# Performance work log

Hardware: AMD Instinct MI355X
Metric: run time of the kernel (lower is better)

Reference implementation:

```python
import jax, jax.numpy as jnp
import numpy as np

DIM, DEPTH, DH, H, NLAT, MAXT, MAXF, FFM = 1024, 6, 64, 8, 64, 8, 16, 4
INNER = DH * H

def _ln(x, w, b, eps=1e-5):
    m = jnp.mean(x, axis=-1, keepdims=True)
    v = jnp.mean(jnp.square(x - m), axis=-1, keepdims=True)
    return (x - m) * jax.lax.rsqrt(v + eps) * w + b

def setup_inputs() -> dict:
    key = jax.random.key(0)
    ks = iter(jax.random.split(key, 32))
    s = 0.02
    d = {
        'x': jax.random.normal(next(ks), (2, 8, 16, 256, DIM), jnp.float32),
        'latents': jax.random.normal(next(ks), (NLAT, DIM), jnp.float32),
        'frame_emb': jax.random.normal(next(ks), (MAXF, DIM), jnp.float32),
        'media_emb': jax.random.normal(next(ks), (MAXT, 1, DIM), jnp.float32),
        'lnm_w': jnp.ones((DEPTH, DIM)), 'lnm_b': jnp.zeros((DEPTH, DIM)),
        'lnl_w': jnp.ones((DEPTH, DIM)), 'lnl_b': jnp.zeros((DEPTH, DIM)),
        'Wq': jax.random.normal(next(ks), (DEPTH, DIM, INNER), jnp.float32) * s,
        'Wkv': jax.random.normal(next(ks), (DEPTH, DIM, 2 * INNER), jnp.float32) * s,
        'Wo': jax.random.normal(next(ks), (DEPTH, INNER, DIM), jnp.float32) * s,
        'ffln_w': jnp.ones((DEPTH, DIM)), 'ffln_b': jnp.zeros((DEPTH, DIM)),
        'W1': jax.random.normal(next(ks), (DEPTH, DIM, FFM * DIM), jnp.float32) * s,
        'b1': jnp.zeros((DEPTH, FFM * DIM)),
        'W2': jax.random.normal(next(ks), (DEPTH, FFM * DIM, DIM), jnp.float32) * s,
        'b2': jnp.zeros((DEPTH, DIM)),
        'fln_w': jnp.ones((DIM,)), 'fln_b': jnp.zeros((DIM,)),
    }
    return d

def _split_heads(t):  # b T n (h d) -> b h T n d
    b, T, n, _ = t.shape
    return t.reshape(b, T, n, H, DH).transpose(0, 3, 1, 2, 4)

def _forward(x, latents, frame_emb, media_emb, lnm_w, lnm_b, lnl_w, lnl_b,
             Wq, Wkv, Wo, ffln_w, ffln_b, W1, b1, W2, b2, fln_w, fln_b):
    b, T, F, v, d = x.shape
    x = x + frame_emb[:F][None, None, :, None, :]      # b T F v d
    x = x.reshape(b, T, F * v, d)
    x = x + media_emb[:T]                              # [T,1,d] broadcasts
    lat = jnp.broadcast_to(latents, (b, T, NLAT, d))
    scale = DH ** -0.5
    for i in range(DEPTH):
        xn = _ln(x, lnm_w[i], lnm_b[i])
        ln_lat = _ln(lat, lnl_w[i], lnl_b[i])
        q = _split_heads(ln_lat @ Wq[i]) * scale       # b h T n2 dh
        kv = jnp.concatenate([xn, ln_lat], axis=2) @ Wkv[i]
        k, vv = jnp.split(kv, 2, axis=-1)
        k, vv = _split_heads(k), _split_heads(vv)      # b h T (n1+n2) dh
        sim = jnp.einsum('bhtid,bhtjd->bhtij', q, k)
        sim = sim - jax.lax.stop_gradient(jnp.max(sim, axis=-1, keepdims=True))
        attn = jax.nn.softmax(sim, axis=-1)
        o = jnp.einsum('bhtij,bhtjd->bhtid', attn, vv)
        o = o.transpose(0, 2, 3, 1, 4).reshape(b, T, NLAT, INNER)
        lat = (o @ Wo[i]) + lat
        h = _ln(lat, ffln_w[i], ffln_b[i])
        h = jax.nn.gelu(h @ W1[i] + b1[i], approximate=False) @ W2[i] + b2[i]
        lat = h + lat
    return _ln(lat, fln_w, fln_b)

def reference(x, latents, frame_emb, media_emb, lnm_w, lnm_b, lnl_w, lnl_b,
              Wq, Wkv, Wo, ffln_w, ffln_b, W1, b1, W2, b2, fln_w, fln_b):
    return _forward(x, latents, frame_emb, media_emb, lnm_w, lnm_b, lnl_w, lnl_b,
                    Wq, Wkv, Wo, ffln_w, ffln_b, W1, b1, W2, b2, fln_w, fln_b)
```

## Files before the change

kernel.cpp:

```cpp
#include <hip/hip_runtime.h>
#include <math.h>


#define DIM   1024
#define DEPTH 6
#define HEADS 8
#define NLAT  64
#define INNER 512
#define FFD   4096
#define XROWS 65536
#define LROWS 1024
#define NBT   16
#define QKVN  1536

typedef __attribute__((ext_vector_type(8))) short bf16x8;
typedef __attribute__((ext_vector_type(4))) float f32x4;

#define WAITV(n) asm volatile("s_waitcnt vmcnt(" #n ")" ::: "memory")

__device__ __forceinline__ short f2bf(float f) {
  union { float f; unsigned u; } v; v.f = f;
  unsigned r = v.u + 0x7fffu + ((v.u >> 16) & 1u);
  return (short)(r >> 16);
}

__device__ __forceinline__ void gload16(const void* g, void* l) {
  __builtin_amdgcn_global_load_lds(
      (const __attribute__((address_space(1))) unsigned int*)g,
      (__attribute__((address_space(3))) unsigned int*)l, 16, 0, 0);
}

__device__ __forceinline__ f32x4 zero_f4() { f32x4 z; z[0]=0.f; z[1]=0.f; z[2]=0.f; z[3]=0.f; return z; }
__device__ __forceinline__ bf16x8 zero_b8() { bf16x8 z;
#pragma unroll
  for (int e=0;e<8;e++) z[e]=0; return z; }

__global__ __launch_bounds__(256)
void prep_kernel(const float* __restrict__ x, const float* __restrict__ fe,
                 const float* __restrict__ me, short* __restrict__ xhat)
{
  int lane = threadIdx.x & 63;
  int r = blockIdx.x*4 + (threadIdx.x >> 6);
  int f = (r >> 8) & 15, tt = (r >> 12) & 7;
  const float4* xp = (const float4*)(x + (size_t)r*DIM);
  const float4* fp = (const float4*)(fe + (size_t)f*DIM);
  const float4* mp = (const float4*)(me + (size_t)tt*DIM);
  float y[16];
  float s = 0.f, sq = 0.f;
#pragma unroll
  for (int k = 0; k < 4; k++) {
    float4 xv = xp[k*64 + lane], fv = fp[k*64 + lane], mv = mp[k*64 + lane];
    float a0 = xv.x+fv.x+mv.x, a1 = xv.y+fv.y+mv.y, a2 = xv.z+fv.z+mv.z, a3 = xv.w+fv.w+mv.w;
    y[k*4+0]=a0; y[k*4+1]=a1; y[k*4+2]=a2; y[k*4+3]=a3;
    s += a0+a1+a2+a3; sq += a0*a0+a1*a1+a2*a2+a3*a3;
  }
#pragma unroll
  for (int off = 32; off >= 1; off >>= 1) {
    s  += __shfl_xor(s,  off, 64);
    sq += __shfl_xor(sq, off, 64);
  }
  float mean = s * (1.0f/DIM);
  float var  = sq * (1.0f/DIM) - mean*mean;
  float rs = rsqrtf(var + 1e-5f);
  short4* op = (short4*)(xhat + (size_t)r*DIM);
#pragma unroll
  for (int k = 0; k < 4; k++) {
    short4 o;
    o.x = f2bf((y[k*4+0]-mean)*rs); o.y = f2bf((y[k*4+1]-mean)*rs);
    o.z = f2bf((y[k*4+2]-mean)*rs); o.w = f2bf((y[k*4+3]-mean)*rs);
    op[k*64 + lane] = o;
  }
}

__device__ __forceinline__ void reduce2(float& s, float& sq, float* sh) {
#pragma unroll
  for (int off = 32; off >= 1; off >>= 1) {
    s  += __shfl_xor(s,  off, 64);
    sq += __shfl_xor(sq, off, 64);
  }
  int t = threadIdx.x;
  if ((t & 63) == 0) { sh[(t >> 6)*2] = s; sh[(t >> 6)*2 + 1] = sq; }
  __syncthreads();
  s  = sh[0] + sh[2] + sh[4] + sh[6];
  sq = sh[1] + sh[3] + sh[5] + sh[7];
}

template<bool OBF>
__global__ __launch_bounds__(256)
void ln_kernel(const float* __restrict__ in, const float* __restrict__ w,
               const float* __restrict__ b, void* __restrict__ outp)
{
  __shared__ float sh[8];
  int r = blockIdx.x, t = threadIdx.x;
  float4 xv = ((const float4*)(in + (size_t)r*DIM))[t];
  float s = xv.x+xv.y+xv.z+xv.w;
  float sq = xv.x*xv.x+xv.y*xv.y+xv.z*xv.z+xv.w*xv.w;
  reduce2(s, sq, sh);
  float mean = s*(1.0f/DIM), var = sq*(1.0f/DIM) - mean*mean;
  float rs = rsqrtf(var + 1e-5f);
  float4 wv = ((const float4*)w)[t], bv = ((const float4*)b)[t];
  float o0 = (xv.x-mean)*rs*wv.x + bv.x;
  float o1 = (xv.y-mean)*rs*wv.y + bv.y;
  float o2 = (xv.z-mean)*rs*wv.z + bv.z;
  float o3 = (xv.w-mean)*rs*wv.w + bv.w;
  if (OBF) {
    short4 o; o.x=f2bf(o0); o.y=f2bf(o1); o.z=f2bf(o2); o.w=f2bf(o3);
    ((short4*)((short*)outp + (size_t)r*DIM))[t] = o;
  } else {
    float4 o; o.x=o0; o.y=o1; o.z=o2; o.w=o3;
    ((float4*)((float*)outp + (size_t)r*DIM))[t] = o;
  }
}

__global__ __launch_bounds__(256)
void latinit_ln_kernel(const float* __restrict__ latents, const float* __restrict__ w,
                       const float* __restrict__ b, float* __restrict__ lat,
                       short* __restrict__ lnlat)
{
  __shared__ float sh[8];
  int r = blockIdx.x, t = threadIdx.x;
  int i = r & 63;
  float4 a = ((const float4*)(latents + (size_t)i*DIM))[t];
  ((float4*)(lat + (size_t)r*DIM))[t] = a;
  float s = a.x+a.y+a.z+a.w;
  float sq = a.x*a.x+a.y*a.y+a.z*a.z+a.w*a.w;
  reduce2(s, sq, sh);
  float mean = s*(1.0f/DIM), var = sq*(1.0f/DIM) - mean*mean;
  float rs = rsqrtf(var + 1e-5f);
  float4 wv = ((const float4*)w)[t], bv = ((const float4*)b)[t];
  short4 o;
  o.x = f2bf((a.x-mean)*rs*wv.x + bv.x);
  o.y = f2bf((a.y-mean)*rs*wv.y + bv.y);
  o.z = f2bf((a.z-mean)*rs*wv.z + bv.z);
  o.w = f2bf((a.w-mean)*rs*wv.w + bv.w);
  ((short4*)(lnlat + (size_t)r*DIM))[t] = o;
}

__global__ __launch_bounds__(256)
void kvbp_kernel(const float* __restrict__ lnm_b, const float* __restrict__ Wkv,
                 float* __restrict__ kvb_part)
{
  int z = blockIdx.x, i = blockIdx.y, t = threadIdx.x;
  const float* W = Wkv + (size_t)i*DIM*DIM;
  const float* bv = lnm_b + (size_t)i*DIM;
  float acc0=0,acc1=0,acc2=0,acc3=0;
  for (int k = z*64; k < z*64+64; k++) {
    float b = bv[k];
    const float* Wr = W + (size_t)k*DIM;
    acc0 += b * Wr[t];       acc1 += b * Wr[t+256];
    acc2 += b * Wr[t+512];   acc3 += b * Wr[t+768];
  }
  float* o = kvb_part + (size_t)(i*16 + z)*DIM;
  o[t] = acc0; o[t+256] = acc1; o[t+512] = acc2; o[t+768] = acc3;
}

__global__ __launch_bounds__(256)
void kvbred_kernel(const float* __restrict__ kvb_part, float* __restrict__ kvb)
{
  int i = blockIdx.x, t = threadIdx.x;
#pragma unroll
  for (int j = 0; j < 4; j++) {
    int col = t + j*256;
    float s = 0.f;
#pragma unroll
    for (int z = 0; z < 16; z++) s += kvb_part[(size_t)(i*16 + z)*DIM + col];
    kvb[i*DIM + col] = s;
  }
}

__global__ __launch_bounds__(256)
void tcast_all_kernel(const float* __restrict__ Wkv, const float* __restrict__ Wq,
                      const float* __restrict__ Wo, const float* __restrict__ W1,
                      const float* __restrict__ W2, const float* __restrict__ lnmw,
                      short* __restrict__ Wkv_f, short* __restrict__ qkvW,
                      short* __restrict__ Wo_h, short* __restrict__ W1_h,
                      short* __restrict__ W2_h)
{
  int b = blockIdx.x;
  const float* src; short* dst; const float* fold = nullptr; float scale = 1.0f;
  int K, N, bx, ntx;
  if (b < 256)      { src=Wkv; dst=Wkv_f; fold=lnmw; K=1024; N=1024; bx=b;      ntx=16; }
  else if (b < 384) { src=Wq;  dst=qkvW;  scale=0.125f; K=1024; N=512; bx=b-256; ntx=8; }
  else if (b < 640) { src=Wkv; dst=qkvW+512*1024; K=1024; N=1024; bx=b-384; ntx=16; }
  else if (b < 768) { src=Wo;  dst=Wo_h;  K=512;  N=1024; bx=b-640; ntx=16; }
  else if (b < 1792){ src=W1;  dst=W1_h;  K=1024; N=4096; bx=b-768; ntx=64; }
  else              { src=W2;  dst=W2_h;  K=4096; N=1024; bx=b-1792; ntx=16; }
  int n0 = (bx % ntx)*64, k0 = (bx / ntx)*64;
  __shared__ float tile[64][65];
  int t = threadIdx.x;
#pragma unroll
  for (int i = 0; i < 16; i++) {
    int rr = (t >> 6) + i*4, cc = t & 63;
    float v = src[(size_t)(k0+rr)*N + n0 + cc] * scale;
    if (fold) v *= fold[k0 + rr];
    tile[rr][cc] = v;
  }
  __syncthreads();
#pragma unroll
  for (int i = 0; i < 16; i++) {
    int nn = (t >> 6) + i*4, kk = t & 63;
    dst[(size_t)(n0+nn)*K + k0 + kk] = f2bf(tile[kk][nn]);
  }
}

__global__ __launch_bounds__(512, 1)
void gemm256p_kernel(const short* __restrict__ A, const short* __restrict__ Bt,
                     short* __restrict__ C, const float* __restrict__ bias,
                     int M, int N, int K)
{
  __shared__ __align__(16) short lds[65536];
  char* ldsc = (char*)lds;
  const int t = threadIdx.x, lane = t & 63, wid = t >> 6;
  const int wm = wid >> 2, wn = wid & 3;

  const int nwg = gridDim.x * gridDim.y;
  const int id = blockIdx.y * gridDim.x + blockIdx.x;
  const int work = (id & 7) * (nwg >> 3) + (id >> 3);
  const int bn = work % gridDim.x, bm = work / gridDim.x;
  const int m0 = bm * 256, n0 = bn * 256;

  f32x4 acc[8][4];
#pragma unroll
  for (int m=0;m<8;m++)
#pragma unroll
    for (int n=0;n<4;n++) acc[m][n] = zero_f4();

  const int hK = K << 7;
  const short* pA[2]; const short* pB[2]; int ldst[2];
#pragma unroll
  for (int i = 0; i < 2; i++) {
    int chunk = i*512 + t;
    int rh = chunk >> 3, sl = chunk & 7;
    int ss = sl ^ (rh & 7);
    pA[i] = A + (size_t)(m0 + rh)*K + ss*8;
    pB[i] = Bt + (size_t)(n0 + rh)*K + ss*8;
    ldst[i] = (i*512 + (wid << 6))*16;
  }
  auto stage = [&](int tile, int mat, int half) {
    char* dbase = ldsc + mat*65536 + (tile & 1)*32768 + half*16384;
#pragma unroll
    for (int i = 0; i < 2; i++) {
      const short* src = (mat ? pB[i] : pA[i]) + half*hK + tile*64;
      gload16(src, dbase + ldst[i]);
    }
  };

  const int sk0 = (((lane >> 4)    ) ^ (lane & 7)) * 16;
  const int sk1 = ((4 + (lane >> 4)) ^ (lane & 7)) * 16;
  const int rowb = (lane & 15) * 128;
  const char* aB[2] = { ldsc + wm*16384 + rowb + sk0, ldsc + wm*16384 + rowb + sk1 };
  const char* bB[2] = { ldsc + 65536 + wn*8192 + rowb + sk0, ldsc + 65536 + wn*8192 + rowb + sk1 };

#define PHASE(BUF, Q, STAGE_STMT, GATE) do {                               \
    if ((Q) == 0) {                                                        \
      _Pragma("unroll") for (int n_=0;n_<4;n_++)                           \
        _Pragma("unroll") for (int k_=0;k_<2;k_++)                         \
          bfr[n_][k_] = *(const bf16x8*)(bB[k_] + (BUF)*32768 + n_*2048);  \
    }                                                                      \
    _Pragma("unroll") for (int i_=0;i_<2;i_++)                             \
      _Pragma("unroll") for (int k_=0;k_<2;k_++)                           \
        afr[i_][k_] = *(const bf16x8*)(aB[k_] + (BUF)*32768 + (2*(Q)+i_)*2048); \
    STAGE_STMT;                                                            \
    GATE;                                                                  \
    __builtin_amdgcn_sched_barrier(0);                                     \
    __builtin_amdgcn_s_barrier();                                          \
    asm volatile("s_waitcnt lgkmcnt(0)" ::: "memory");                     \
    __builtin_amdgcn_sched_barrier(0);                                     \
    __builtin_amdgcn_s_setprio(1);                                         \
    _Pragma("unroll") for (int k_=0;k_<2;k_++)                             \
      _Pragma("unroll") for (int i_=0;i_<2;i_++)                           \
        _Pragma("unroll") for (int n_=0;n_<4;n_++)                         \
          acc[2*(Q)+i_][n_] = __builtin_amdgcn_mfma_f32_16x16x32_bf16(     \
              afr[i_][k_], bfr[n_][k_], acc[2*(Q)+i_][n_], 0, 0, 0);       \
    __builtin_amdgcn_s_setprio(0);                                         \
    __builtin_amdgcn_sched_barrier(0);                                     \
    __builtin_amdgcn_s_barrier();                                          \
  } while (0)

  const int NU = K >> 7;
  stage(0, 0, 0); stage(0, 0, 1); stage(0, 1, 0); stage(0, 1, 1);
  stage(1, 1, 0); stage(1, 1, 1);
  WAITV(4);
  __builtin_amdgcn_sched_barrier(0);
  __builtin_amdgcn_s_barrier();

#pragma unroll 1
  for (int u = 0; u < NU; ++u) {
    const int t0 = 2*u, t1 = t0 + 1;
    const bool more = (u + 1 < NU);
    bf16x8 bfr[4][2], afr[2][2];
    PHASE(0, 0, stage(t1, 0, 0),               (void)0);
    PHASE(0, 1, stage(t1, 0, 1),               (void)0);
    PHASE(0, 2, if (more) stage(t0+2, 1, 0),   (void)0);
    PHASE(0, 3, if (more) stage(t0+2, 1, 1),   if (more) { WAITV(4); } else { WAITV(0); });
    PHASE(1, 0, if (more) stage(t0+2, 0, 0),   (void)0);
    PHASE(1, 1, if (more) stage(t0+2, 0, 1),   (void)0);
    PHASE(1, 2, if (more) stage(t1+2, 1, 0),   (void)0);
    PHASE(1, 3, if (more) stage(t1+2, 1, 1),   if (more) { WAITV(4); });
  }
#undef PHASE

  const int g = lane >> 4;
#pragma unroll
  for (int m=0;m<8;m++) {
#pragma unroll
    for (int n=0;n<4;n++) {
#pragma unroll
      for (int r=0;r<4;r++) {
        int mm = m0 + wm*128 + m*16 + g*4 + r;
        int nn = n0 + wn*64 + n*16 + (lane & 15);
        float v = acc[m][n][r] + bias[nn];
        C[(size_t)mm*N + nn] = f2bf(v);
      }
    }
  }
}

template<int EPI, bool HAS_BIAS>
__global__ __launch_bounds__(256, 2)
void gemm_kernel(const short* __restrict__ A, const short* __restrict__ Bt,
                 void* __restrict__ Cout, const float* __restrict__ bias,
                 int M, int N, int K, int ldk)
{
  __shared__ __align__(16) short As[128*64];
  __shared__ __align__(16) short Bs[128*64];
  const int t = threadIdx.x;
  const int lane = t & 63, w = t >> 6;
  const int m0 = blockIdx.x * 128, n0 = blockIdx.y * 128;
  const int wr = (w >> 1) * 64, wc = (w & 1) * 64;
  const short* Ap = A + (size_t)blockIdx.z * K;
  const short* Btp = Bt + (size_t)blockIdx.z * K;

  f32x4 acc[4][4];
#pragma unroll
  for (int i=0;i<4;i++)
#pragma unroll
    for (int j=0;j<4;j++) acc[i][j] = zero_f4();

  for (int kt = 0; kt < K; kt += 64) {
#pragma unroll
    for (int i = 0; i < 4; i++) {
      int chunk = i*256 + t;
      int row = chunk >> 3, slot = chunk & 7;
      int ss = slot ^ (row & 7);
      gload16(Ap + (size_t)(m0 + row)*ldk + kt + ss*8,
              (char*)As + (i*256 + (w<<6))*16);
    }
#pragma unroll
    for (int i = 0; i < 4; i++) {
      int chunk = i*256 + t;
      int row = chunk >> 3, slot = chunk & 7;
      int ss = slot ^ (row & 7);
      gload16(Btp + (size_t)(n0 + row)*ldk + kt + ss*8,
              (char*)Bs + (i*256 + (w<<6))*16);
    }
    __syncthreads();

#pragma unroll
    for (int ks = 0; ks < 2; ks++) {
      bf16x8 af[4], bfr[4];
#pragma unroll
      for (int i=0;i<4;i++) {
        int row = wr + i*16 + (lane & 15);
        int slot = (ks*4 + (lane >> 4)) ^ (row & 7);
        af[i] = *(const bf16x8*)((const char*)As + row*128 + slot*16);
        int nrow = wc + i*16 + (lane & 15);
        int nslot = (ks*4 + (lane >> 4)) ^ (nrow & 7);
        bfr[i] = *(const bf16x8*)((const char*)Bs + nrow*128 + nslot*16);
      }
#pragma unroll
      for (int i=0;i<4;i++)
#pragma unroll
        for (int j=0;j<4;j++)
          acc[i][j] = __builtin_amdgcn_mfma_f32_16x16x32_bf16(af[i], bfr[j], acc[i][j], 0, 0, 0);
    }
    __syncthreads();
  }

  const int g = lane >> 4;
#pragma unroll
  for (int i=0;i<4;i++) {
#pragma unroll
    for (int j=0;j<4;j++) {
#pragma unroll
      for (int r=0;r<4;r++) {
        int m = m0 + wr + i*16 + g*4 + r;
        int n = n0 + wc + j*16 + (lane & 15);
        float v = acc[i][j][r];
        if (EPI == 0) {
          if (HAS_BIAS) v += bias[n];
          ((short*)Cout)[(size_t)m*N + n] = f2bf(v);
        } else if (EPI == 1) {
          if (HAS_BIAS) v += bias[n];
          float gl = 0.5f * v * (1.0f + erff(v * 0.70710678f));
          ((short*)Cout)[(size_t)m*N + n] = f2bf(gl);
        } else if (EPI == 2) {
          if (HAS_BIAS) v += bias[n];
          float* o = (float*)Cout + (size_t)m*N + n;
          *o += v;
        } else {
          ((float*)Cout)[(size_t)blockIdx.z*M*N + (size_t)m*N + n] = v;
        }
      }
    }
  }
}

template<bool LAST>
__global__ __launch_bounds__(256)
void w2red_ln_kernel(const float* __restrict__ part, const float* __restrict__ b2,
                     float* __restrict__ lat, const float* __restrict__ w,
                     const float* __restrict__ bb, void* __restrict__ dst)
{
  __shared__ float sh[8];
  int r = blockIdx.x, t = threadIdx.x;
  int idx = r*256 + t;
  float4 a = ((float4*)lat)[idx];
  float4 b4 = ((const float4*)b2)[t];
  a.x += b4.x; a.y += b4.y; a.z += b4.z; a.w += b4.w;
#pragma unroll
  for (int z = 0; z < 4; z++) {
    float4 p = ((const float4*)(part + (size_t)z*LROWS*DIM))[idx];
    a.x += p.x; a.y += p.y; a.z += p.z; a.w += p.w;
  }
  ((float4*)lat)[idx] = a;
  float s = a.x+a.y+a.z+a.w;
  float sq = a.x*a.x+a.y*a.y+a.z*a.z+a.w*a.w;
  reduce2(s, sq, sh);
  float mean = s*(1.0f/DIM), var = sq*(1.0f/DIM) - mean*mean;
  float rs = rsqrtf(var + 1e-5f);
  float4 wv = ((const float4*)w)[t], bv = ((const float4*)bb)[t];
  float o0 = (a.x-mean)*rs*wv.x + bv.x;
  float o1 = (a.y-mean)*rs*wv.y + bv.y;
  float o2 = (a.z-mean)*rs*wv.z + bv.z;
  float o3 = (a.w-mean)*rs*wv.w + bv.w;
  if (LAST) {
    float4 o; o.x=o0; o.y=o1; o.z=o2; o.w=o3;
    ((float4*)((float*)dst + (size_t)r*DIM))[t] = o;
  } else {
    short4 o; o.x=f2bf(o0); o.y=f2bf(o1); o.z=f2bf(o2); o.w=f2bf(o3);
    ((short4*)((short*)dst + (size_t)r*DIM))[t] = o;
  }
}

__global__ __launch_bounds__(256, 2)
void attn_part_kernel(const short* __restrict__ qkvlat, const short* __restrict__ kvbuf,
                      float* __restrict__ part_O, float* __restrict__ part_m,
                      float* __restrict__ part_l)
{
  __shared__ __align__(16) short q_sh[64*64];
  __shared__ __align__(16) short K_sh[128*64];
  __shared__ __align__(16) short VT_sh[64*128];
  __shared__ __align__(16) short P_sh[64*132];

  const int t = threadIdx.x, lane = t & 63, w = t >> 6;
  const int bid = blockIdx.x;
  const int s = bid & 7, bh = bid >> 3;
  const int h = bh & 7, bt = bh >> 3;

  {
    const short* qsrc = qkvlat + (size_t)(bt*64)*QKVN + h*64;
#pragma unroll
    for (int i = 0; i < 2; i++) {
      int chunk = i*256 + t;
      int row = chunk >> 3, slot = chunk & 7;
      gload16(qsrc + (size_t)row*QKVN + ((slot ^ (row & 7))*8),
              (char*)q_sh + (i*256 + (w<<6))*16);
    }
  }

  float m_run[4], l_run[4];
#pragma unroll
  for (int r=0;r<4;r++){ m_run[r] = -1e30f; l_run[r] = 0.f; }
  f32x4 oacc[4];
#pragma unroll
  for (int j=0;j<4;j++) oacc[j] = zero_f4();

  const int nch = (s == 7) ? 5 : 4;
  for (int c5 = 0; c5 < nch; c5++) {
    __syncthreads();
    const bool isLat = (c5 == 4);
    const int jv = isLat ? 4 : 8;
    const short* kbase; int kstride, valid;
    if (!isLat) {
      kbase = kvbuf + ((size_t)bt*4096 + (s*4 + c5)*128)*DIM + h*64;
      kstride = DIM; valid = 128;
    } else {
      kbase = qkvlat + (size_t)(bt*64)*QKVN + 512 + h*64;
// ... 106 lines not shown
    for (int j=0;j<4;j++) {
#pragma unroll
      for (int r=0;r<4;r++)
        Ob[(rbase + r)*64 + j*16 + (lane & 15)] = oacc[j][r];
    }
    if ((lane & 15) == 0) {
#pragma unroll
      for (int r=0;r<4;r++) {
        part_m[(size_t)bid*64 + rbase + r] = m_run[r];
        part_l[(size_t)bid*64 + rbase + r] = l_run[r];
      }
    }
  }
}

__global__ __launch_bounds__(256)
void attn_combine_kernel(const float* __restrict__ part_O, const float* __restrict__ part_m,
                         const float* __restrict__ part_l, short* __restrict__ obuf)
{
  int bh = blockIdx.x, t = threadIdx.x;
  int q = t >> 2, c0 = (t & 3) * 16;
  int bt = bh >> 3, h = bh & 7;
  float m8[8], w8[8];
  float mmax = -1e30f;
#pragma unroll
  for (int s=0;s<8;s++) { m8[s] = part_m[(size_t)(bh*8+s)*64 + q]; mmax = fmaxf(mmax, m8[s]); }
  float lt = 0.f;
#pragma unroll
  for (int s=0;s<8;s++) { w8[s] = __expf(m8[s] - mmax); lt += w8[s] * part_l[(size_t)(bh*8+s)*64 + q]; }
  float inv = 1.0f / lt;
  float4 acc[4];
#pragma unroll
  for (int u=0;u<4;u++) { acc[u].x=0.f; acc[u].y=0.f; acc[u].z=0.f; acc[u].w=0.f; }
#pragma unroll
  for (int s=0;s<8;s++) {
    const float4* Ob = (const float4*)(part_O + ((size_t)(bh*8+s)*64 + q)*64 + c0);
#pragma unroll
    for (int u=0;u<4;u++) {
      float4 v = Ob[u];
      acc[u].x += w8[s]*v.x; acc[u].y += w8[s]*v.y;
      acc[u].z += w8[s]*v.z; acc[u].w += w8[s]*v.w;
    }
  }
  short* ob = obuf + (size_t)(bt*64 + q)*INNER + h*64 + c0;
#pragma unroll
  for (int u=0;u<4;u++) {
    short4 o;
    o.x = f2bf(acc[u].x*inv); o.y = f2bf(acc[u].y*inv);
    o.z = f2bf(acc[u].z*inv); o.w = f2bf(acc[u].w*inv);
    ((short4*)ob)[u] = o;
  }
}

extern "C" void kernel_launch(void* const* d_in, const int* in_sizes, int n_in,
                              void* d_out, int out_size, void* d_ws, size_t ws_size,
                              hipStream_t stream)
{
  (void)in_sizes; (void)n_in; (void)out_size; (void)ws_size;
  const float* x        = (const float*)d_in[0];
  const float* latents  = (const float*)d_in[1];
  const float* frame_e  = (const float*)d_in[2];
  const float* media_e  = (const float*)d_in[3];
  const float* lnm_w    = (const float*)d_in[4];
  const float* lnm_b    = (const float*)d_in[5];
  const float* lnl_w    = (const float*)d_in[6];
  const float* lnl_b    = (const float*)d_in[7];
  const float* Wq       = (const float*)d_in[8];
  const float* Wkv      = (const float*)d_in[9];
  const float* Wo       = (const float*)d_in[10];
  const float* ffln_w   = (const float*)d_in[11];
  const float* ffln_b   = (const float*)d_in[12];
  const float* W1       = (const float*)d_in[13];
  const float* b1       = (const float*)d_in[14];
  const float* W2       = (const float*)d_in[15];
  const float* b2       = (const float*)d_in[16];
  const float* fln_w    = (const float*)d_in[17];
  const float* fln_b    = (const float*)d_in[18];
  float* out = (float*)d_out;

  char* ws = (char*)d_ws;
  size_t off = 0;
  short* xhat   = (short*)(ws + off); off += (size_t)XROWS*DIM*2;
  short* kvbuf  = (short*)(ws + off); off += (size_t)XROWS*DIM*2;
  short* Wkv_f  = (short*)(ws + off); off += (size_t)DIM*DIM*2;
  short* qkvW   = (short*)(ws + off); off += (size_t)QKVN*DIM*2;
  short* Wo_h   = (short*)(ws + off); off += (size_t)INNER*DIM*2;
  short* W1_h   = (short*)(ws + off); off += (size_t)DIM*FFD*2;
  short* W2_h   = (short*)(ws + off); off += (size_t)FFD*DIM*2;
  float* kvb    = (float*)(ws + off); off += (size_t)DEPTH*DIM*4;
  float* kvbp   = (float*)(ws + off); off += (size_t)DEPTH*16*DIM*4;
  float* lat    = (float*)(ws + off); off += (size_t)LROWS*DIM*4;
  short* lnlat  = (short*)(ws + off); off += (size_t)LROWS*DIM*2;
  short* qkvlat = (short*)(ws + off); off += (size_t)LROWS*QKVN*2;
  short* obuf   = (short*)(ws + off); off += (size_t)LROWS*INNER*2;
  short* hbuf   = (short*)(ws + off); off += (size_t)LROWS*DIM*2;
  short* h1     = (short*)(ws + off); off += (size_t)LROWS*FFD*2;
  float* w2part = (float*)(ws + off); off += (size_t)4*LROWS*DIM*4;
  float* part_O = (float*)(ws + off); off += (size_t)1024*64*64*4;
  float* part_m = (float*)(ws + off); off += (size_t)1024*64*4;
  float* part_l = (float*)(ws + off); off += (size_t)1024*64*4;

  prep_kernel<<<XROWS/4, 256, 0, stream>>>(x, frame_e, media_e, xhat);
  latinit_ln_kernel<<<LROWS, 256, 0, stream>>>(latents, lnl_w, lnl_b, lat, lnlat);
  kvbp_kernel<<<dim3(16, DEPTH), 256, 0, stream>>>(lnm_b, Wkv, kvbp);
  kvbred_kernel<<<DEPTH, 256, 0, stream>>>(kvbp, kvb);

  for (int i = 0; i < DEPTH; i++) {
    tcast_all_kernel<<<2816, 256, 0, stream>>>(
        Wkv + (size_t)i*DIM*DIM, Wq + (size_t)i*DIM*INNER, Wo + (size_t)i*INNER*DIM,
        W1 + (size_t)i*DIM*FFD, W2 + (size_t)i*FFD*DIM, lnm_w + (size_t)i*DIM,
        Wkv_f, qkvW, Wo_h, W1_h, W2_h);

    gemm_kernel<0,false><<<dim3(LROWS/128, QKVN/128), 256, 0, stream>>>(
        lnlat, qkvW, qkvlat, nullptr, LROWS, QKVN, DIM, DIM);
    gemm256p_kernel<<<dim3(DIM/256, XROWS/256), 512, 0, stream>>>(
        xhat, Wkv_f, kvbuf, kvb + i*DIM, XROWS, DIM, DIM);
    attn_part_kernel<<<1024, 256, 0, stream>>>(qkvlat, kvbuf, part_O, part_m, part_l);
    attn_combine_kernel<<<128, 256, 0, stream>>>(part_O, part_m, part_l, obuf);
    gemm_kernel<2,false><<<dim3(LROWS/128, DIM/128), 256, 0, stream>>>(
        obuf, Wo_h, lat, nullptr, LROWS, DIM, INNER, INNER);
    ln_kernel<true><<<LROWS, 256, 0, stream>>>(lat, ffln_w + i*DIM, ffln_b + i*DIM, hbuf);
    gemm_kernel<1,true><<<dim3(LROWS/128, FFD/128), 256, 0, stream>>>(
        hbuf, W1_h, h1, b1 + (size_t)i*FFD, LROWS, FFD, DIM, DIM);
    gemm_kernel<4,false><<<dim3(LROWS/128, DIM/128, 4), 256, 0, stream>>>(
        h1, W2_h, w2part, nullptr, LROWS, DIM, DIM, FFD);
    if (i < DEPTH-1)
      w2red_ln_kernel<false><<<LROWS, 256, 0, stream>>>(
          w2part, b2 + (size_t)i*DIM, lat, lnl_w + (i+1)*DIM, lnl_b + (i+1)*DIM, lnlat);
    else
      w2red_ln_kernel<true><<<LROWS, 256, 0, stream>>>(
          w2part, b2 + (size_t)i*DIM, lat, fln_w, fln_b, out);
  }
}
```

Measured before the change: 2.077 ms.

## Double-buffer LDS fragment registers to overlap LDS reads with MFMA in GEMM

Restructures the GEMM main loop so the A and B fragments are ping-ponged between two register sets. The reads for the next phase are issued before the current phase's MFMAs, and the lgkmcnt waits are partial instead of full, so LDS read latency can hide behind matrix math. The WAITV gating is also moved earlier in the pipeline. In exchange, register pressure rises, the waitcnt accounting is subtle, and a miscount could race with the buffer stage writes.

```diff
diff --git a/kernel.cpp b/kernel.cpp
--- a/kernel.cpp
+++ b/kernel.cpp
@@ -248,33 +248,38 @@
   const int sk0 = (((lane >> 4)    ) ^ (lane & 7)) * 16;
   const int sk1 = ((4 + (lane >> 4)) ^ (lane & 7)) * 16;
   const int rowb = (lane & 15) * 128;
-  const char* aB[2] = { ldsc + wm*16384 + rowb + sk0, ldsc + wm*16384 + rowb + sk1 };
-  const char* bB[2] = { ldsc + 65536 + wn*8192 + rowb + sk0, ldsc + 65536 + wn*8192 + rowb + sk1 };
-
-#define PHASE(BUF, Q, STAGE_STMT, GATE) do {                               \
-    if ((Q) == 0) {                                                        \
-      _Pragma("unroll") for (int n_=0;n_<4;n_++)                           \
-        _Pragma("unroll") for (int k_=0;k_<2;k_++)                         \
-          bfr[n_][k_] = *(const bf16x8*)(bB[k_] + (BUF)*32768 + n_*2048);  \
-    }                                                                      \
-    _Pragma("unroll") for (int i_=0;i_<2;i_++)                             \
-      _Pragma("unroll") for (int k_=0;k_<2;k_++)                           \
-        afr[i_][k_] = *(const bf16x8*)(aB[k_] + (BUF)*32768 + (2*(Q)+i_)*2048); \
-    STAGE_STMT;                                                            \
-    GATE;                                                                  \
-    __builtin_amdgcn_sched_barrier(0);                                     \
-    __builtin_amdgcn_s_barrier();                                          \
-    asm volatile("s_waitcnt lgkmcnt(0)" ::: "memory");                     \
-    __builtin_amdgcn_sched_barrier(0);                                     \
-    __builtin_amdgcn_s_setprio(1);                                         \
-    _Pragma("unroll") for (int k_=0;k_<2;k_++)                             \
-      _Pragma("unroll") for (int i_=0;i_<2;i_++)                           \
-        _Pragma("unroll") for (int n_=0;n_<4;n_++)                         \
-          acc[2*(Q)+i_][n_] = __builtin_amdgcn_mfma_f32_16x16x32_bf16(     \
-              afr[i_][k_], bfr[n_][k_], acc[2*(Q)+i_][n_], 0, 0, 0);       \
-    __builtin_amdgcn_s_setprio(0);                                         \
-    __builtin_amdgcn_sched_barrier(0);                                     \
-    __builtin_amdgcn_s_barrier();                                          \
+  const char* aLB[2] = { ldsc + wm*16384 + rowb + sk0, ldsc + wm*16384 + rowb + sk1 };
+  const char* bLB[2] = { ldsc + 65536 + wn*8192 + rowb + sk0, ldsc + 65536 + wn*8192 + rowb + sk1 };
+
+  bf16x8 aA[2][2], aB[2][2];
+  bf16x8 bC[4][2], bN[4][2];
+
+#define RD_A(DST, BUF, Q)                                                   \
+  { _Pragma("unroll") for (int i_=0;i_<2;i_++)                              \
+      _Pragma("unroll") for (int k_=0;k_<2;k_++)                            \
+        DST[i_][k_] = *(const bf16x8*)(aLB[k_] + (BUF)*32768 + (2*(Q)+i_)*2048); }
+#define RD_B2(DST, BUF, N0)                                                 \
+  { _Pragma("unroll") for (int n_=0;n_<2;n_++)                              \
+      _Pragma("unroll") for (int k_=0;k_<2;k_++)                            \
+        DST[(N0)+n_][k_] = *(const bf16x8*)(bLB[k_] + (BUF)*32768 + ((N0)+n_)*2048); }
+
+#define PHASE(AF, BF, Q, READS, STAGE_STMT, GATE, LGKM) do {                \
+    READS;                                                                  \
+    STAGE_STMT;                                                             \
+    GATE;                                                                   \
+    __builtin_amdgcn_sched_barrier(0);                                      \
+    __builtin_amdgcn_s_barrier();                                           \
+    asm volatile("s_waitcnt lgkmcnt(" #LGKM ")" ::: "memory");              \
+    __builtin_amdgcn_sched_barrier(0);                                      \
+    __builtin_amdgcn_s_setprio(1);                                          \
+    _Pragma("unroll") for (int k_=0;k_<2;k_++)                              \
+      _Pragma("unroll") for (int i_=0;i_<2;i_++)                            \
+        _Pragma("unroll") for (int n_=0;n_<4;n_++)                          \
+          acc[2*(Q)+i_][n_] = __builtin_amdgcn_mfma_f32_16x16x32_bf16(      \
+              AF[i_][k_], BF[n_][k_], acc[2*(Q)+i_][n_], 0, 0, 0);          \
+    __builtin_amdgcn_s_setprio(0);                                          \
+    __builtin_amdgcn_sched_barrier(0);                                      \
+    __builtin_amdgcn_s_barrier();                                           \
   } while (0)
 
   const int NU = K >> 7;
@@ -283,22 +288,28 @@
   WAITV(4);
   __builtin_amdgcn_sched_barrier(0);
   __builtin_amdgcn_s_barrier();
+  RD_B2(bC, 0, 0); RD_B2(bC, 0, 2);
+  __builtin_amdgcn_sched_barrier(0);
 
 #pragma unroll 1
   for (int u = 0; u < NU; ++u) {
     const int t0 = 2*u, t1 = t0 + 1;
     const bool more = (u + 1 < NU);
-    bf16x8 bfr[4][2], afr[2][2];
-    PHASE(0, 0, stage(t1, 0, 0),               (void)0);
-    PHASE(0, 1, stage(t1, 0, 1),               (void)0);
-    PHASE(0, 2, if (more) stage(t0+2, 1, 0),   (void)0);
-    PHASE(0, 3, if (more) stage(t0+2, 1, 1),   if (more) { WAITV(4); } else { WAITV(0); });
-    PHASE(1, 0, if (more) stage(t0+2, 0, 0),   (void)0);
-    PHASE(1, 1, if (more) stage(t0+2, 0, 1),   (void)0);
-    PHASE(1, 2, if (more) stage(t1+2, 1, 0),   (void)0);
-    PHASE(1, 3, if (more) stage(t1+2, 1, 1),   if (more) { WAITV(4); });
+    PHASE(aA, bC, 0, { RD_A(aA,0,0); RD_A(aB,0,1); }, stage(t1,0,0), (void)0, 4);
+    PHASE(aB, bC, 1, { RD_A(aA,0,2); },               stage(t1,0,1), WAITV(4), 4);
+    PHASE(aA, bC, 2, { RD_A(aB,0,3); RD_B2(bN,1,0); }, if (more) stage(t0+2,1,0), (void)0, 8);
+    PHASE(aB, bC, 3, { RD_B2(bN,1,2); },               if (more) stage(t0+2,1,1),
+          if (more) { WAITV(4); } else { WAITV(0); }, 8);
+    PHASE(aA, bN, 0, { RD_A(aA,1,0); RD_A(aB,1,1); }, if (more) stage(t0+2,0,0), (void)0, 4);
+    PHASE(aB, bN, 1, { RD_A(aA,1,2); },               if (more) stage(t0+2,0,1),
+          if (more) { WAITV(4); }, 4);
+    PHASE(aA, bN, 2, { RD_A(aB,1,3); RD_B2(bC,0,0); }, if (more) stage(t1+2,1,0), (void)0, 8);
+    PHASE(aB, bN, 3, { RD_B2(bC,0,2); },               if (more) stage(t1+2,1,1),
+          if (more) { WAITV(4); }, 8);
   }
 #undef PHASE
+#undef RD_A
+#undef RD_B2
 
   const int g = lane >> 4;
 #pragma unroll
```

Result: no change. 2.096 ms (+0.9%).

## Make big KV GEMM persistent over N-tiles and batch weight casts

Applied to the files above, without the earlier changes.

The large x-by-Wkv GEMM now launches 256 blocks, each owning a 256-row M stripe. Each block walks all four 256-wide N tiles in one continuous K pipeline, writing and resetting its accumulators every 16 k-steps. This keeps the A stripe hot in cache and removes the per-tile prologue and epilogue pipeline drains. Separately, the six per-layer weight transpose/cast launches are merged into one upfront launch writing per-layer buffers. This costs more workspace, and w2part now aliases the part_O buffer.

```diff
diff --git a/kernel.cpp b/kernel.cpp
--- a/kernel.cpp
+++ b/kernel.cpp
@@ -169,22 +169,24 @@
 }
 
 __global__ __launch_bounds__(256)
-void tcast_all_kernel(const float* __restrict__ Wkv, const float* __restrict__ Wq,
-                      const float* __restrict__ Wo, const float* __restrict__ W1,
-                      const float* __restrict__ W2, const float* __restrict__ lnmw,
-                      short* __restrict__ Wkv_f, short* __restrict__ qkvW,
-                      short* __restrict__ Wo_h, short* __restrict__ W1_h,
-                      short* __restrict__ W2_h)
-{
-  int b = blockIdx.x;
+void tcast_all6_kernel(const float* __restrict__ Wkv, const float* __restrict__ Wq,
+                       const float* __restrict__ Wo, const float* __restrict__ W1,
+                       const float* __restrict__ W2, const float* __restrict__ lnm_w,
+                       short* __restrict__ Wkvf_a, short* __restrict__ qkvW_a,
+                       short* __restrict__ Wo_a, short* __restrict__ W1_a,
+                       short* __restrict__ W2_a)
+{
+  int L = blockIdx.x / 2816;
+  int b = blockIdx.x % 2816;
+  const float* lWkv = Wkv + (size_t)L*DIM*DIM;
   const float* src; short* dst; const float* fold = nullptr; float scale = 1.0f;
   int K, N, bx, ntx;
-  if (b < 256)      { src=Wkv; dst=Wkv_f; fold=lnmw; K=1024; N=1024; bx=b;      ntx=16; }
-  else if (b < 384) { src=Wq;  dst=qkvW;  scale=0.125f; K=1024; N=512; bx=b-256; ntx=8; }
-  else if (b < 640) { src=Wkv; dst=qkvW+512*1024; K=1024; N=1024; bx=b-384; ntx=16; }
-  else if (b < 768) { src=Wo;  dst=Wo_h;  K=512;  N=1024; bx=b-640; ntx=16; }
-  else if (b < 1792){ src=W1;  dst=W1_h;  K=1024; N=4096; bx=b-768; ntx=64; }
-  else              { src=W2;  dst=W2_h;  K=4096; N=1024; bx=b-1792; ntx=16; }
+  if (b < 256)      { src=lWkv; dst=Wkvf_a + (size_t)L*DIM*DIM; fold=lnm_w + (size_t)L*DIM; K=1024; N=1024; bx=b; ntx=16; }
+  else if (b < 384) { src=Wq + (size_t)L*DIM*INNER; dst=qkvW_a + (size_t)L*QKVN*DIM; scale=0.125f; K=1024; N=512; bx=b-256; ntx=8; }
+  else if (b < 640) { src=lWkv; dst=qkvW_a + (size_t)L*QKVN*DIM + (size_t)512*1024; K=1024; N=1024; bx=b-384; ntx=16; }
+  else if (b < 768) { src=Wo + (size_t)L*INNER*DIM; dst=Wo_a + (size_t)L*INNER*DIM; K=512;  N=1024; bx=b-640; ntx=16; }
+  else if (b < 1792){ src=W1 + (size_t)L*DIM*FFD; dst=W1_a + (size_t)L*DIM*FFD; K=1024; N=4096; bx=b-768; ntx=64; }
+  else              { src=W2 + (size_t)L*FFD*DIM; dst=W2_a + (size_t)L*FFD*DIM; K=4096; N=1024; bx=b-1792; ntx=16; }
   int n0 = (bx % ntx)*64, k0 = (bx / ntx)*64;
   __shared__ float tile[64][65];
   int t = threadIdx.x;
@@ -204,20 +206,18 @@
 }
 
 __global__ __launch_bounds__(512, 1)
-void gemm256p_kernel(const short* __restrict__ A, const short* __restrict__ Bt,
-                     short* __restrict__ C, const float* __restrict__ bias,
-                     int M, int N, int K)
+void gemm256pp_kernel(const short* __restrict__ A, const short* __restrict__ Bt,
+                      short* __restrict__ C, const float* __restrict__ bias)
 {
   __shared__ __align__(16) short lds[65536];
   char* ldsc = (char*)lds;
   const int t = threadIdx.x, lane = t & 63, wid = t >> 6;
   const int wm = wid >> 2, wn = wid & 3;
-
-  const int nwg = gridDim.x * gridDim.y;
-  const int id = blockIdx.y * gridDim.x + blockIdx.x;
-  const int work = (id & 7) * (nwg >> 3) + (id >> 3);
-  const int bn = work % gridDim.x, bm = work / gridDim.x;
-  const int m0 = bm * 256, n0 = bn * 256;
+  const int K = DIM, N = DIM;
+
+  const int b = blockIdx.x;
+  const int bm = (b & 7)*32 + (b >> 3);
+  const int m0 = bm * 256;
 
   f32x4 acc[8][4];
 #pragma unroll
@@ -226,21 +226,24 @@
     for (int n=0;n<4;n++) acc[m][n] = zero_f4();
 
   const int hK = K << 7;
-  const short* pA[2]; const short* pB[2]; int ldst[2];
+  const short* pA[2]; const short* pB0[2]; int ldst[2];
 #pragma unroll
   for (int i = 0; i < 2; i++) {
     int chunk = i*512 + t;
     int rh = chunk >> 3, sl = chunk & 7;
     int ss = sl ^ (rh & 7);
-    pA[i] = A + (size_t)(m0 + rh)*K + ss*8;
-    pB[i] = Bt + (size_t)(n0 + rh)*K + ss*8;
+    pA[i]  = A + (size_t)(m0 + rh)*K + ss*8;
+    pB0[i] = Bt + (size_t)rh*K + ss*8;
     ldst[i] = (i*512 + (wid << 6))*16;
   }
-  auto stage = [&](int tile, int mat, int half) {
-    char* dbase = ldsc + mat*65536 + (tile & 1)*32768 + half*16384;
+  auto stage = [&](int vt, int mat, int half) {
+    char* dbase = ldsc + mat*65536 + (vt & 1)*32768 + half*16384;
+    const int koff = (vt & 15)*64;
+    const size_t bout = (size_t)(vt >> 4)*256*K;
 #pragma unroll
     for (int i = 0; i < 2; i++) {
-      const short* src = (mat ? pB[i] : pA[i]) + half*hK + tile*64;
+      const short* src = mat ? (pB0[i] + bout + half*hK + koff)
+                             : (pA[i] + half*hK + koff);
       gload16(src, dbase + ldst[i]);
     }
   };
@@ -277,43 +280,45 @@
     __builtin_amdgcn_s_barrier();                                          \
   } while (0)
 
-  const int NU = K >> 7;
+  const int NVT = 64;
   stage(0, 0, 0); stage(0, 0, 1); stage(0, 1, 0); stage(0, 1, 1);
   stage(1, 1, 0); stage(1, 1, 1);
   WAITV(4);
   __builtin_amdgcn_sched_barrier(0);
   __builtin_amdgcn_s_barrier();
 
+  const int g = lane >> 4;
 #pragma unroll 1
-  for (int u = 0; u < NU; ++u) {
-    const int t0 = 2*u, t1 = t0 + 1;
-    const bool more = (u + 1 < NU);
+  for (int u = 0; u < 32; ++u) {
+    const int vt0 = 2*u, vt1 = vt0 + 1;
+    const bool more = (vt0 + 2 < NVT);
     bf16x8 bfr[4][2], afr[2][2];
-    PHASE(0, 0, stage(t1, 0, 0),               (void)0);
-    PHASE(0, 1, stage(t1, 0, 1),               (void)0);
-    PHASE(0, 2, if (more) stage(t0+2, 1, 0),   (void)0);
-    PHASE(0, 3, if (more) stage(t0+2, 1, 1),   if (more) { WAITV(4); } else { WAITV(0); });
-    PHASE(1, 0, if (more) stage(t0+2, 0, 0),   (void)0);
-    PHASE(1, 1, if (more) stage(t0+2, 0, 1),   (void)0);
-    PHASE(1, 2, if (more) stage(t1+2, 1, 0),   (void)0);
-    PHASE(1, 3, if (more) stage(t1+2, 1, 1),   if (more) { WAITV(4); });
+    PHASE(0, 0, stage(vt1, 0, 0),               (void)0);
+    PHASE(0, 1, stage(vt1, 0, 1),               (void)0);
+    PHASE(0, 2, if (more) stage(vt0+2, 1, 0),   (void)0);
+    PHASE(0, 3, if (more) stage(vt0+2, 1, 1),   if (more) { WAITV(4); } else { WAITV(0); });
+    PHASE(1, 0, if (more) stage(vt0+2, 0, 0),   (void)0);
+    PHASE(1, 1, if (more) stage(vt0+2, 0, 1),   (void)0);
+    PHASE(1, 2, if (more) stage(vt1+2, 1, 0),   (void)0);
+    PHASE(1, 3, if (more) stage(vt1+2, 1, 1),   if (more) { WAITV(4); });
+    if ((u & 7) == 7) {
+      const int n0 = (u >> 3) * 256;
+#pragma unroll
+      for (int m=0;m<8;m++) {
+#pragma unroll
+        for (int n=0;n<4;n++) {
+#pragma unroll
+          for (int r=0;r<4;r++) {
+            int mm = m0 + wm*128 + m*16 + g*4 + r;
+            int nn = n0 + wn*64 + n*16 + (lane & 15);
+            C[(size_t)mm*N + nn] = f2bf(acc[m][n][r] + bias[nn]);
+          }
+          acc[m][n] = zero_f4();
+        }
+      }
+    }
   }
 #undef PHASE
-
-  const int g = lane >> 4;
-#pragma unroll
-  for (int m=0;m<8;m++) {
-#pragma unroll
-    for (int n=0;n<4;n++) {
-#pragma unroll
-      for (int r=0;r<4;r++) {
-        int mm = m0 + wm*128 + m*16 + g*4 + r;
-        int nn = n0 + wn*64 + n*16 + (lane & 15);
-        float v = acc[m][n][r] + bias[nn];
-        C[(size_t)mm*N + nn] = f2bf(v);
-      }
-    }
-  }
 }
 
 template<int EPI, bool HAS_BIAS>
@@ -676,11 +681,11 @@
   size_t off = 0;
   short* xhat   = (short*)(ws + off); off += (size_t)XROWS*DIM*2;
   short* kvbuf  = (short*)(ws + off); off += (size_t)XROWS*DIM*2;
-  short* Wkv_f  = (short*)(ws + off); off += (size_t)DIM*DIM*2;
-  short* qkvW   = (short*)(ws + off); off += (size_t)QKVN*DIM*2;
-  short* Wo_h   = (short*)(ws + off); off += (size_t)INNER*DIM*2;
-  short* W1_h   = (short*)(ws + off); off += (size_t)DIM*FFD*2;
-  short* W2_h   = (short*)(ws + off); off += (size_t)FFD*DIM*2;
+  short* Wkvf_a = (short*)(ws + off); off += (size_t)DEPTH*DIM*DIM*2;
+  short* qkvW_a = (short*)(ws + off); off += (size_t)DEPTH*QKVN*DIM*2;
+  short* Wo_a   = (short*)(ws + off); off += (size_t)DEPTH*INNER*DIM*2;
+  short* W1_a   = (short*)(ws + off); off += (size_t)DEPTH*DIM*FFD*2;
+  short* W2_a   = (short*)(ws + off); off += (size_t)DEPTH*FFD*DIM*2;
   float* kvb    = (float*)(ws + off); off += (size_t)DEPTH*DIM*4;
   float* kvbp   = (float*)(ws + off); off += (size_t)DEPTH*16*DIM*4;
   float* lat    = (float*)(ws + off); off += (size_t)LROWS*DIM*4;
@@ -689,8 +694,8 @@
   short* obuf   = (short*)(ws + off); off += (size_t)LROWS*INNER*2;
   short* hbuf   = (short*)(ws + off); off += (size_t)LROWS*DIM*2;
   short* h1     = (short*)(ws + off); off += (size_t)LROWS*FFD*2;
-  float* w2part = (float*)(ws + off); off += (size_t)4*LROWS*DIM*4;
   float* part_O = (float*)(ws + off); off += (size_t)1024*64*64*4;
+  float* w2part = part_O;
   float* part_m = (float*)(ws + off); off += (size_t)1024*64*4;
   float* part_l = (float*)(ws + off); off += (size_t)1024*64*4;
 
@@ -698,17 +703,19 @@
   latinit_ln_kernel<<<LROWS, 256, 0, stream>>>(latents, lnl_w, lnl_b, lat, lnlat);
   kvbp_kernel<<<dim3(16, DEPTH), 256, 0, stream>>>(lnm_b, Wkv, kvbp);
   kvbred_kernel<<<DEPTH, 256, 0, stream>>>(kvbp, kvb);
+  tcast_all6_kernel<<<DEPTH*2816, 256, 0, stream>>>(
+      Wkv, Wq, Wo, W1, W2, lnm_w, Wkvf_a, qkvW_a, Wo_a, W1_a, W2_a);
 
   for (int i = 0; i < DEPTH; i++) {
-    tcast_all_kernel<<<2816, 256, 0, stream>>>(
-        Wkv + (size_t)i*DIM*DIM, Wq + (size_t)i*DIM*INNER, Wo + (size_t)i*INNER*DIM,
-        W1 + (size_t)i*DIM*FFD, W2 + (size_t)i*FFD*DIM, lnm_w + (size_t)i*DIM,
-        Wkv_f, qkvW, Wo_h, W1_h, W2_h);
+    const short* Wkv_f = Wkvf_a + (size_t)i*DIM*DIM;
+    const short* qkvW  = qkvW_a + (size_t)i*QKVN*DIM;
+    const short* Wo_h  = Wo_a   + (size_t)i*INNER*DIM;
+    const short* W1_h  = W1_a   + (size_t)i*DIM*FFD;
+    const short* W2_h  = W2_a   + (size_t)i*FFD*DIM;
 
     gemm_kernel<0,false><<<dim3(LROWS/128, QKVN/128), 256, 0, stream>>>(
         lnlat, qkvW, qkvlat, nullptr, LROWS, QKVN, DIM, DIM);
-    gemm256p_kernel<<<dim3(DIM/256, XROWS/256), 512, 0, stream>>>(
-        xhat, Wkv_f, kvbuf, kvb + i*DIM, XROWS, DIM, DIM);
+    gemm256pp_kernel<<<256, 512, 0, stream>>>(xhat, Wkv_f, kvbuf, kvb + i*DIM);
     attn_part_kernel<<<1024, 256, 0, stream>>>(qkvlat, kvbuf, part_O, part_m, part_l);
     attn_combine_kernel<<<128, 256, 0, stream>>>(part_O, part_m, part_l, obuf);
     gemm_kernel<2,false><<<dim3(LROWS/128, DIM/128), 256, 0, stream>>>(
```

Result: slower. 2.192 ms (+5.5%).

## Hoist weight casts for all layers into one launch; split-K Wo with fused LN

Applied to the files above, without the earlier changes.

Weight transpose/cast work for all six layers now runs in a single large launch before the layer loop instead of one launch per layer, with per-layer bf16 weight buffers in the workspace. The Wo projection becomes a 2-way split-K GEMM writing partials. A new kernel sums those partials into the residual and applies the feed-forward LayerNorm in the same pass, replacing the separate accumulate epilogue and LN kernel. This raises parallelism for the small Wo GEMM and removes one launch and one pass over the latents, at the cost of more workspace and a larger upfront cast kernel. The W2 partial buffer now aliases the attention partial buffer.

```diff
diff --git a/kernel.cpp b/kernel.cpp
--- a/kernel.cpp
+++ b/kernel.cpp
@@ -83,33 +83,6 @@
   __syncthreads();
   s  = sh[0] + sh[2] + sh[4] + sh[6];
   sq = sh[1] + sh[3] + sh[5] + sh[7];
-}
-
-template<bool OBF>
-__global__ __launch_bounds__(256)
-void ln_kernel(const float* __restrict__ in, const float* __restrict__ w,
-               const float* __restrict__ b, void* __restrict__ outp)
-{
-  __shared__ float sh[8];
-  int r = blockIdx.x, t = threadIdx.x;
-  float4 xv = ((const float4*)(in + (size_t)r*DIM))[t];
-  float s = xv.x+xv.y+xv.z+xv.w;
-  float sq = xv.x*xv.x+xv.y*xv.y+xv.z*xv.z+xv.w*xv.w;
-  reduce2(s, sq, sh);
-  float mean = s*(1.0f/DIM), var = sq*(1.0f/DIM) - mean*mean;
-  float rs = rsqrtf(var + 1e-5f);
-  float4 wv = ((const float4*)w)[t], bv = ((const float4*)b)[t];
-  float o0 = (xv.x-mean)*rs*wv.x + bv.x;
-  float o1 = (xv.y-mean)*rs*wv.y + bv.y;
-  float o2 = (xv.z-mean)*rs*wv.z + bv.z;
-  float o3 = (xv.w-mean)*rs*wv.w + bv.w;
-  if (OBF) {
-    short4 o; o.x=f2bf(o0); o.y=f2bf(o1); o.z=f2bf(o2); o.w=f2bf(o3);
-    ((short4*)((short*)outp + (size_t)r*DIM))[t] = o;
-  } else {
-    float4 o; o.x=o0; o.y=o1; o.z=o2; o.w=o3;
-    ((float4*)((float*)outp + (size_t)r*DIM))[t] = o;
-  }
 }
 
 __global__ __launch_bounds__(256)
@@ -169,22 +142,24 @@
 }
 
 __global__ __launch_bounds__(256)
-void tcast_all_kernel(const float* __restrict__ Wkv, const float* __restrict__ Wq,
-                      const float* __restrict__ Wo, const float* __restrict__ W1,
-                      const float* __restrict__ W2, const float* __restrict__ lnmw,
-                      short* __restrict__ Wkv_f, short* __restrict__ qkvW,
-                      short* __restrict__ Wo_h, short* __restrict__ W1_h,
-                      short* __restrict__ W2_h)
-{
-  int b = blockIdx.x;
+void tcast_all6_kernel(const float* __restrict__ Wkv, const float* __restrict__ Wq,
+                       const float* __restrict__ Wo, const float* __restrict__ W1,
+                       const float* __restrict__ W2, const float* __restrict__ lnm_w,
+                       short* __restrict__ Wkvf_a, short* __restrict__ qkvW_a,
+                       short* __restrict__ Wo_a, short* __restrict__ W1_a,
+                       short* __restrict__ W2_a)
+{
+  int L = blockIdx.x / 2816;
+  int b = blockIdx.x % 2816;
+  const float* lWkv = Wkv + (size_t)L*DIM*DIM;
   const float* src; short* dst; const float* fold = nullptr; float scale = 1.0f;
   int K, N, bx, ntx;
-  if (b < 256)      { src=Wkv; dst=Wkv_f; fold=lnmw; K=1024; N=1024; bx=b;      ntx=16; }
-  else if (b < 384) { src=Wq;  dst=qkvW;  scale=0.125f; K=1024; N=512; bx=b-256; ntx=8; }
-  else if (b < 640) { src=Wkv; dst=qkvW+512*1024; K=1024; N=1024; bx=b-384; ntx=16; }
-  else if (b < 768) { src=Wo;  dst=Wo_h;  K=512;  N=1024; bx=b-640; ntx=16; }
-  else if (b < 1792){ src=W1;  dst=W1_h;  K=1024; N=4096; bx=b-768; ntx=64; }
-  else              { src=W2;  dst=W2_h;  K=4096; N=1024; bx=b-1792; ntx=16; }
+  if (b < 256)      { src=lWkv; dst=Wkvf_a + (size_t)L*DIM*DIM; fold=lnm_w + (size_t)L*DIM; K=1024; N=1024; bx=b; ntx=16; }
+  else if (b < 384) { src=Wq + (size_t)L*DIM*INNER; dst=qkvW_a + (size_t)L*QKVN*DIM; scale=0.125f; K=1024; N=512; bx=b-256; ntx=8; }
+  else if (b < 640) { src=lWkv; dst=qkvW_a + (size_t)L*QKVN*DIM + (size_t)512*1024; K=1024; N=1024; bx=b-384; ntx=16; }
+  else if (b < 768) { src=Wo + (size_t)L*INNER*DIM; dst=Wo_a + (size_t)L*INNER*DIM; K=512;  N=1024; bx=b-640; ntx=16; }
+  else if (b < 1792){ src=W1 + (size_t)L*DIM*FFD; dst=W1_a + (size_t)L*DIM*FFD; K=1024; N=4096; bx=b-768; ntx=64; }
+  else              { src=W2 + (size_t)L*FFD*DIM; dst=W2_a + (size_t)L*FFD*DIM; K=4096; N=1024; bx=b-1792; ntx=16; }
   int n0 = (bx % ntx)*64, k0 = (bx / ntx)*64;
   __shared__ float tile[64][65];
   int t = threadIdx.x;
@@ -394,16 +369,39 @@
           if (HAS_BIAS) v += bias[n];
           float gl = 0.5f * v * (1.0f + erff(v * 0.70710678f));
           ((short*)Cout)[(size_t)m*N + n] = f2bf(gl);
-        } else if (EPI == 2) {
-          if (HAS_BIAS) v += bias[n];
-          float* o = (float*)Cout + (size_t)m*N + n;
-          *o += v;
         } else {
           ((float*)Cout)[(size_t)blockIdx.z*M*N + (size_t)m*N + n] = v;
         }
       }
     }
   }
+}
+
+__global__ __launch_bounds__(256)
+void wored_ffln_kernel(const float* __restrict__ part, float* __restrict__ lat,
+                       const float* __restrict__ w, const float* __restrict__ bb,
+                       short* __restrict__ hbuf)
+{
+  __shared__ float sh[8];
+  int r = blockIdx.x, t = threadIdx.x;
+  int idx = r*256 + t;
+  float4 a = ((float4*)lat)[idx];
+  float4 p0 = ((const float4*)part)[idx];
+  float4 p1 = ((const float4*)(part + (size_t)LROWS*DIM))[idx];
+  a.x += p0.x + p1.x; a.y += p0.y + p1.y; a.z += p0.z + p1.z; a.w += p0.w + p1.w;
+  ((float4*)lat)[idx] = a;
+  float s = a.x+a.y+a.z+a.w;
+  float sq = a.x*a.x+a.y*a.y+a.z*a.z+a.w*a.w;
+  reduce2(s, sq, sh);
+  float mean = s*(1.0f/DIM), var = sq*(1.0f/DIM) - mean*mean;
+  float rs = rsqrtf(var + 1e-5f);
+  float4 wv = ((const float4*)w)[t], bv = ((const float4*)bb)[t];
+  short4 o;
+  o.x = f2bf((a.x-mean)*rs*wv.x + bv.x);
+  o.y = f2bf((a.y-mean)*rs*wv.y + bv.y);
+  o.z = f2bf((a.z-mean)*rs*wv.z + bv.z);
+  o.w = f2bf((a.w-mean)*rs*wv.w + bv.w);
+  ((short4*)(hbuf + (size_t)r*DIM))[t] = o;
 }
 
 template<bool LAST>
@@ -676,11 +674,11 @@
   size_t off = 0;
   short* xhat   = (short*)(ws + off); off += (size_t)XROWS*DIM*2;
   short* kvbuf  = (short*)(ws + off); off += (size_t)XROWS*DIM*2;
-  short* Wkv_f  = (short*)(ws + off); off += (size_t)DIM*DIM*2;
-  short* qkvW   = (short*)(ws + off); off += (size_t)QKVN*DIM*2;
-  short* Wo_h   = (short*)(ws + off); off += (size_t)INNER*DIM*2;
-  short* W1_h   = (short*)(ws + off); off += (size_t)DIM*FFD*2;
-  short* W2_h   = (short*)(ws + off); off += (size_t)FFD*DIM*2;
+  short* Wkvf_a = (short*)(ws + off); off += (size_t)DEPTH*DIM*DIM*2;
+  short* qkvW_a = (short*)(ws + off); off += (size_t)DEPTH*QKVN*DIM*2;
+  short* Wo_a   = (short*)(ws + off); off += (size_t)DEPTH*INNER*DIM*2;
+  short* W1_a   = (short*)(ws + off); off += (size_t)DEPTH*DIM*FFD*2;
+  short* W2_a   = (short*)(ws + off); off += (size_t)DEPTH*FFD*DIM*2;
   float* kvb    = (float*)(ws + off); off += (size_t)DEPTH*DIM*4;
   float* kvbp   = (float*)(ws + off); off += (size_t)DEPTH*16*DIM*4;
   float* lat    = (float*)(ws + off); off += (size_t)LROWS*DIM*4;
@@ -689,8 +687,9 @@
   short* obuf   = (short*)(ws + off); off += (size_t)LROWS*INNER*2;
   short* hbuf   = (short*)(ws + off); off += (size_t)LROWS*DIM*2;
   short* h1     = (short*)(ws + off); off += (size_t)LROWS*FFD*2;
-  float* w2part = (float*)(ws + off); off += (size_t)4*LROWS*DIM*4;
+  float* wopart = (float*)(ws + off); off += (size_t)2*LROWS*DIM*4;
   float* part_O = (float*)(ws + off); off += (size_t)1024*64*64*4;
+  float* w2part = part_O;
   float* part_m = (float*)(ws + off); off += (size_t)1024*64*4;
   float* part_l = (float*)(ws + off); off += (size_t)1024*64*4;
 
@@ -698,12 +697,15 @@
   latinit_ln_kernel<<<LROWS, 256, 0, stream>>>(latents, lnl_w, lnl_b, lat, lnlat);
   kvbp_kernel<<<dim3(16, DEPTH), 256, 0, stream>>>(lnm_b, Wkv, kvbp);
   kvbred_kernel<<<DEPTH, 256, 0, stream>>>(kvbp, kvb);
+  tcast_all6_kernel<<<DEPTH*2816, 256, 0, stream>>>(
+      Wkv, Wq, Wo, W1, W2, lnm_w, Wkvf_a, qkvW_a, Wo_a, W1_a, W2_a);
 
   for (int i = 0; i < DEPTH; i++) {
-    tcast_all_kernel<<<2816, 256, 0, stream>>>(
-        Wkv + (size_t)i*DIM*DIM, Wq + (size_t)i*DIM*INNER, Wo + (size_t)i*INNER*DIM,
-        W1 + (size_t)i*DIM*FFD, W2 + (size_t)i*FFD*DIM, lnm_w + (size_t)i*DIM,
-        Wkv_f, qkvW, Wo_h, W1_h, W2_h);
+    const short* Wkv_f = Wkvf_a + (size_t)i*DIM*DIM;
+    const short* qkvW  = qkvW_a + (size_t)i*QKVN*DIM;
+    const short* Wo_h  = Wo_a   + (size_t)i*INNER*DIM;
+    const short* W1_h  = W1_a   + (size_t)i*DIM*FFD;
+    const short* W2_h  = W2_a   + (size_t)i*FFD*DIM;
 
     gemm_kernel<0,false><<<dim3(LROWS/128, QKVN/128), 256, 0, stream>>>(
         lnlat, qkvW, qkvlat, nullptr, LROWS, QKVN, DIM, DIM);
@@ -711,9 +713,10 @@
         xhat, Wkv_f, kvbuf, kvb + i*DIM, XROWS, DIM, DIM);
     attn_part_kernel<<<1024, 256, 0, stream>>>(qkvlat, kvbuf, part_O, part_m, part_l);
     attn_combine_kernel<<<128, 256, 0, stream>>>(part_O, part_m, part_l, obuf);
-    gemm_kernel<2,false><<<dim3(LROWS/128, DIM/128), 256, 0, stream>>>(
-        obuf, Wo_h, lat, nullptr, LROWS, DIM, INNER, INNER);
-    ln_kernel<true><<<LROWS, 256, 0, stream>>>(lat, ffln_w + i*DIM, ffln_b + i*DIM, hbuf);
+    gemm_kernel<4,false><<<dim3(LROWS/128, DIM/128, 2), 256, 0, stream>>>(
+        obuf, Wo_h, wopart, nullptr, LROWS, DIM, 256, INNER);
+    wored_ffln_kernel<<<LROWS, 256, 0, stream>>>(
+        wopart, lat, ffln_w + i*DIM, ffln_b + i*DIM, hbuf);
     gemm_kernel<1,true><<<dim3(LROWS/128, FFD/128), 256, 0, stream>>>(
         hbuf, W1_h, h1, b1 + (size_t)i*FFD, LROWS, FFD, DIM, DIM);
     gemm_kernel<4,false><<<dim3(LROWS/128, DIM/128, 4), 256, 0, stream>>>(
```

Measured after the change: 1.953 ms. 1.06x faster.
